# Performance work log

Hardware: AMD Instinct MI355X
Metric: run time of the kernel (lower is better)

Reference implementation:

```python
import jax, jax.numpy as jnp
import numpy as np

N, NB, D, F, E, NUM_RBF = 50000, 256, 128, 16, 800000, 15
EPS = 1e-7
NEG = 0.01
MAX_LEN = 5.0


def _glorot(k, shape):
    return jax.random.normal(k, shape, dtype=jnp.float32) / np.float32(np.sqrt(shape[0]))


def setup_inputs() -> dict:
    key = jax.random.key(0)
    ks = jax.random.split(key, 32)
    inp = {}
    inp['h_A'] = jax.random.normal(ks[0], (N, D), jnp.float32)
    inp['v_A'] = jax.random.normal(ks[1], (N, F, 3), jnp.float32)
    inp['x_A'] = jax.random.normal(ks[2], (N, 3), jnp.float32) * 3.0
    inp['h_B'] = jax.random.normal(ks[3], (NB, D), jnp.float32)
    inp['mask'] = jnp.ones((N, NB), jnp.float32)
    inp['src'] = jax.random.randint(ks[4], (E,), 0, N, dtype=jnp.int32)
    inp['dst'] = jax.random.randint(ks[5], (E,), 0, N, dtype=jnp.int32)
    inp['rbf_k'] = jnp.array([0.5], jnp.float32)
    inp['W_rbf1'] = _glorot(ks[6], (NUM_RBF, D)); inp['b_rbf1'] = jnp.zeros((D,), jnp.float32)
    inp['W_rbf2'] = _glorot(ks[7], (NUM_RBF, F)); inp['b_rbf2'] = jnp.zeros((F,), jnp.float32)
    inp['W_rbf3'] = _glorot(ks[8], (NUM_RBF, F)); inp['b_rbf3'] = jnp.zeros((F,), jnp.float32)
    inp['vn1_W'] = _glorot(ks[9], (F, F)); inp['vn1_U'] = _glorot(ks[10], (F, F))
    inp['vn2_W'] = _glorot(ks[11], (F, F)); inp['vn2_U'] = _glorot(ks[12], (F, F))
    inp['vn3_W'] = _glorot(ks[13], (F, F)); inp['vn3_U'] = _glorot(ks[14], (F, F))
    inp['phi1_W'] = _glorot(ks[15], (D + F, D)); inp['phi1_b'] = jnp.zeros((D,), jnp.float32)
    inp['phi2_W'] = _glorot(ks[16], (D + F, F)); inp['phi2_b'] = jnp.zeros((F,), jnp.float32)
    inp['phi3_W'] = _glorot(ks[17], (D, F)); inp['phi3_b'] = jnp.zeros((F,), jnp.float32)
    inp['Wq'] = _glorot(ks[18], (D, D)); inp['Wk'] = _glorot(ks[19], (D, D))
    inp['Wv'] = _glorot(ks[20], (D, D)); inp['bv'] = jnp.zeros((D,), jnp.float32)
    inp['gru_Wih'] = _glorot(ks[21], (3 * D, 2 * D)) * 0.5
    inp['gru_Whh'] = _glorot(ks[22], (3 * D, D)) * 0.5
    inp['gru_bih'] = jnp.zeros((3 * D,), jnp.float32)
    inp['gru_bhh'] = jnp.zeros((3 * D,), jnp.float32)
    inp['vmlp_W1'] = _glorot(ks[23], (2 * F, 2 * F)); inp['vmlp_U1'] = _glorot(ks[24], (2 * F, 2 * F))
    inp['vmlp_W2'] = _glorot(ks[25], (F, 2 * F))
    return inp


def _forward(h_A, v_A, x_A, h_B, mask, src, dst, rbf_k, W_rbf1, b_rbf1, W_rbf2, b_rbf2,
             W_rbf3, b_rbf3, vn1_W, vn1_U, vn2_W, vn2_U, vn3_W, vn3_U, phi1_W, phi1_b,
             phi2_W, phi2_b, phi3_W, phi3_b, Wq, Wk, Wv, bv, gru_Wih, gru_Whh, gru_bih,
             gru_bhh, vmlp_W1, vmlp_U1, vmlp_W2):
    lrelu = lambda x: jax.nn.leaky_relu(x, NEG)

    def vn_relu(v, W, U):  # Vector Neuron linear + VN-ReLU; v: [n, f, 3]
        q = jnp.einsum('gf,nfc->ngc', W, v)
        k = jnp.einsum('gf,nfc->ngc', U, v)
        dot = jnp.sum(q * k, -1, keepdims=True)
        ksq = jnp.sum(k * k, -1, keepdims=True) + EPS
        return jnp.where(dot >= 0, q, q - (dot / ksq) * k)

    # --- per-node mixed scalar/vector features (generate_mixed_features) ---
    vnorm1 = jnp.linalg.norm(vn_relu(v_A, vn1_W, vn1_U), axis=2) + EPS  # [N,F]
    vnorm2 = jnp.linalg.norm(vn_relu(v_A, vn2_W, vn2_U), axis=2) + EPS
    hp = lrelu(jnp.concatenate([h_A, vnorm1], 1) @ phi1_W + phi1_b)     # [N,D]
    hpp = lrelu(jnp.concatenate([h_A, vnorm2], 1) @ phi2_W + phi2_b)    # [N,F]
    vp = vn_relu(v_A, vn3_W, vn3_U) * lrelu(h_A @ phi3_W + phi3_b)[:, :, None]  # [N,F,3]

    # --- cross attention A <- B ---
    q = lrelu(h_A @ Wq)
    kk = lrelu(h_B @ Wk)
    vv = h_B @ Wv + bv
    a = mask * (q @ kk.T) - 1000.0 * (1.0 - mask)                       # [N,NB]
    attn = jax.nn.softmax(a, axis=1) @ vv                               # [N,D]

    # --- edge-wise RBF expansion + point convolution messages ---
    r_ij = x_A[src] - x_A[dst]                                          # [E,3]
    rnorm = jnp.linalg.norm(r_ij, axis=1, keepdims=True)                # [E,1]
    centers = jnp.linspace(0.0, MAX_LEN, NUM_RBF, dtype=jnp.float32)
    rbf = jnp.exp(-jnp.square(rnorm - centers) * rbf_k)                 # [E,R]
    rbf_h = rbf @ W_rbf1 + b_rbf1                                       # [E,D]
    rbf_v1 = rbf @ W_rbf2 + b_rbf2                                      # [E,F]
    rbf_v2 = rbf @ W_rbf3 + b_rbf3                                      # [E,F]
    msg_h = rbf_h * hp[dst]                                             # [E,D]
    # einsum('ef,ef,ec->efc', rbf_v2, hpp_dst, r_ij)
    msg_v = rbf_v1[:, :, None] * vp[dst] + (rbf_v2 * hpp[dst])[:, :, None] * r_ij[:, None, :]

    # --- mean aggregation at destination nodes (update_all copy_e + mean) ---
    n_nodes = h_A.shape[0]
    cnt = jax.ops.segment_sum(jnp.ones((src.shape[0],), msg_h.dtype), dst, num_segments=n_nodes)
    den = jnp.maximum(cnt, 1.0)
    agg_h = jax.ops.segment_sum(msg_h, dst, num_segments=n_nodes) / den[:, None]
    agg_v = jax.ops.segment_sum(msg_v, dst, num_segments=n_nodes) / den[:, None, None]

    # --- GRUCell(2D, D): input = [h, cross_attn], hidden = aggregated message ---
    x_in = jnp.concatenate([h_A, attn], -1)                             # [N,2D]
    gi = x_in @ gru_Wih.T + gru_bih
    gh = agg_h @ gru_Whh.T + gru_bhh
    Dh = h_A.shape[1]
    r = jax.nn.sigmoid(gi[:, :Dh] + gh[:, :Dh])
    z = jax.nn.sigmoid(gi[:, Dh:2 * Dh] + gh[:, Dh:2 * Dh])
    n = jnp.tanh(gi[:, 2 * Dh:] + r * gh[:, 2 * Dh:])
    node_upd = h_A + ((1.0 - z) * n + z * agg_h)

    # --- vector update via Vector_MLP(2F -> F) with residual ---
    vin = jnp.concatenate([v_A, agg_v], axis=1)                         # [N,2F,3]
    vh = vn_relu(vin, vmlp_W1, vmlp_U1)
    v_evolved = v_A + jnp.einsum('gf,nfc->ngc', vmlp_W2, vh)            # [N,F,3]
    return v_evolved, node_upd


def reference(h_A, v_A, x_A, h_B, mask, src, dst, rbf_k, W_rbf1, b_rbf1, W_rbf2, b_rbf2,
              W_rbf3, b_rbf3, vn1_W, vn1_U, vn2_W, vn2_U, vn3_W, vn3_U, phi1_W, phi1_b,
              phi2_W, phi2_b, phi3_W, phi3_b, Wq, Wk, Wv, bv, gru_Wih, gru_Whh, gru_bih,
              gru_bhh, vmlp_W1, vmlp_U1, vmlp_W2):
    return _forward(h_A, v_A, x_A, h_B, mask, src, dst, rbf_k, W_rbf1, b_rbf1, W_rbf2,
                    b_rbf2, W_rbf3, b_rbf3, vn1_W, vn1_U, vn2_W, vn2_U, vn3_W, vn3_U,
                    phi1_W, phi1_b, phi2_W, phi2_b, phi3_W, phi3_b, Wq, Wk, Wv, bv,
                    gru_Wih, gru_Whh, gru_bih, gru_bhh, vmlp_W1, vmlp_U1, vmlp_W2)
```

## Files before the change

kernel.cpp:

```cpp
#include <hip/hip_runtime.h>
#include <math.h>

#define NN 50000
#define NBB 256
#define DD 128
#define FF 16
#define EE 800000
#define RR 15
#define EPSV 1e-7f
#define CSPACE (5.0f/14.0f)

__device__ __forceinline__ float lrelu(float x){ return x >= 0.f ? x : 0.01f*x; }
__device__ __forceinline__ float sigmoidf_(float x){ return 1.f/(1.f+expf(-x)); }

typedef __bf16 bf16x8 __attribute__((ext_vector_type(8)));
typedef float f32x4 __attribute__((ext_vector_type(4)));

__device__ __forceinline__ unsigned short f2bf(float x){
    union { float f; unsigned int u; } a; a.f = x;
    unsigned int r = (a.u + 0x7fffu + ((a.u >> 16) & 1u)) >> 16;
    return (unsigned short)r;
}
__device__ __forceinline__ unsigned int pack2(float a, float b){
    return (unsigned int)f2bf(a) | ((unsigned int)f2bf(b) << 16);
}
__device__ __forceinline__ float bf2f(unsigned short v){
    union { unsigned int u; float f; } a; a.u = ((unsigned int)v) << 16; return a.f;
}
__device__ __forceinline__ bf16x8 ld8(const unsigned short* p){
    union { uint4 u; bf16x8 b; } x; x.u = *(const uint4*)p; return x.b;
}

__global__ void k_prep(const float* __restrict__ Wih, const float* __restrict__ Whh,
                       const float* __restrict__ Wq,
                       const float* __restrict__ phi1W, const float* __restrict__ phi2W,
                       const float* __restrict__ phi3W,
                       unsigned short* __restrict__ pWih, unsigned short* __restrict__ pWhh,
                       unsigned short* __restrict__ pWq,
                       unsigned short* __restrict__ pPhi1, unsigned short* __restrict__ pPhi2,
                       unsigned short* __restrict__ pPhi3){
    int i = blockIdx.x*256 + threadIdx.x;
    if (i < 3*8*8*64*8){
        int e = i&7, l=(i>>3)&63, kt=(i>>9)&7, c=(i>>12)&7, q=i>>15;
        int row = q*128 + c*16 + (l&15);
        int k = kt*32 + (l>>4)*8 + e;
        pWih[i] = f2bf(Wih[row*256 + k]);
    }
    if (i < 3*8*4*64*8){
        int e = i&7, l=(i>>3)&63, kt=(i>>9)&3, c=(i>>11)&7, q=i>>14;
        int row = q*128 + c*16 + (l&15);
        int k = kt*32 + (l>>4)*8 + e;
        pWhh[i] = f2bf(Whh[row*128 + k]);
    }
    if (i < 8*4*64*8){
        int e = i&7, l=(i>>3)&63, kt=(i>>9)&3, c=(i>>11)&7;
        pWq[i] = f2bf(Wq[(kt*32 + (l>>4)*8 + e)*DD + c*16 + (l&15)]);
    }
    if (i < 8*5*64*8){
        int e = i&7, l=(i>>3)&63;
        int t = i>>9;
        int kt = t%5, c = t/5;
        int k = kt*32 + (l>>4)*8 + e;
        int col = c*16 + (l&15);
        pPhi1[i] = f2bf(k < 144 ? phi1W[k*DD + col] : 0.f);
    }
    if (i < 5*64*8){
        int e = i&7, l=(i>>3)&63, kt = i>>9;
        int k = kt*32 + (l>>4)*8 + e;
        int col = l&15;
        pPhi2[i] = f2bf(k < 144 ? phi2W[k*FF + col] : 0.f);
    }
    if (i < 4*64*8){
        int e = i&7, l=(i>>3)&63, kt = i>>9;
        int k = kt*32 + (l>>4)*8 + e;
        int col = l&15;
        pPhi3[i] = f2bf(phi3W[k*FF + col]);
    }
}

__global__ __launch_bounds__(512) void k_node(
    const float* __restrict__ hA, const float* __restrict__ vA,
    const float* __restrict__ vn1W, const float* __restrict__ vn1U,
    const float* __restrict__ vn2W, const float* __restrict__ vn2U,
    const float* __restrict__ vn3W, const float* __restrict__ vn3U,
    const unsigned short* __restrict__ pPhi1, const float* __restrict__ phi1b,
    const unsigned short* __restrict__ pPhi2, const float* __restrict__ phi2b,
    const unsigned short* __restrict__ pPhi3, const float* __restrict__ phi3b,
    float* __restrict__ hpO, float* __restrict__ hppO, float* __restrict__ vpO)
{
    __shared__ unsigned short sH[64*128];
    __shared__ unsigned short sE[64*64];
    __shared__ float sVA[64*48];
    __shared__ float sO3[64*16*3];
    __shared__ float sW[6*256];
    int tid = threadIdx.x;
    int n0 = blockIdx.x*64;

    #pragma unroll
    for (int it = 0; it < 2; ++it){
        int c = tid + it*512;
        int row = c >> 4, cb = c & 15;
        int gn = n0 + row; if (gn > NN-1) gn = NN-1;
        const float* p = hA + (size_t)gn*DD + cb*8;
        float4 f0 = *(const float4*)p;
        float4 f1 = *(const float4*)(p+4);
        uint4 u;
        u.x = pack2(f0.x,f0.y); u.y = pack2(f0.z,f0.w);
        u.z = pack2(f1.x,f1.y); u.w = pack2(f1.z,f1.w);
        *(uint4*)&sH[row*128 + ((cb ^ (row&7))*8)] = u;
    }
    #pragma unroll
    for (int it = 0; it < 6; ++it){
        int i = tid + it*512;
        int row = i/48, cc = i%48;
        int gn = n0 + row; if (gn > NN-1) gn = NN-1;
        sVA[i] = vA[(size_t)gn*48 + cc];
    }
    #pragma unroll
    for (int it = 0; it < 3; ++it){
        int i = tid + it*512;
        float v;
        if      (i <  256) v = vn1W[i];
        else if (i <  512) v = vn1U[i-256];
        else if (i <  768) v = vn2W[i-512];
        else if (i < 1024) v = vn2U[i-768];
        else if (i < 1280) v = vn3W[i-1024];
        else               v = vn3U[i-1280];
        sW[i] = v;
    }
    {
        uint2* z = (uint2*)sE;
        z[tid] = make_uint2(0u,0u);
        z[tid+512] = make_uint2(0u,0u);
    }
    __syncthreads();

    #pragma unroll
    for (int it = 0; it < 2; ++it){
        int item = tid + it*512;
        int nl = item >> 4, g = item & 15;
        const float* v = &sVA[nl*48];
        float q0[3]={0,0,0}, q1[3]={0,0,0}, q2[3]={0,0,0};
        float c0[3]={0,0,0}, c1[3]={0,0,0}, c2[3]={0,0,0};
        #pragma unroll
        for (int ff = 0; ff < FF; ++ff){
            int fi = (ff + g) & 15;
            float v0 = v[fi*3], v1 = v[fi*3+1], v2 = v[fi*3+2];
            #pragma unroll
            for (int m = 0; m < 3; ++m){
                float w = sW[m*512 + g*16 + fi];
                float u = sW[m*512 + 256 + g*16 + fi];
                q0[m] += w*v0; q1[m] += w*v1; q2[m] += w*v2;
                c0[m] += u*v0; c1[m] += u*v1; c2[m] += u*v2;
            }
        }
        #pragma unroll
        for (int m = 0; m < 3; ++m){
            float dot = q0[m]*c0[m] + q1[m]*c1[m] + q2[m]*c2[m];
            float ksq = c0[m]*c0[m] + c1[m]*c1[m] + c2[m]*c2[m] + EPSV;
            float s = dot >= 0.f ? 0.f : dot/ksq;
            float o0 = q0[m]-s*c0[m], o1 = q1[m]-s*c1[m], o2 = q2[m]-s*c2[m];
            if (m < 2){
                float nr = sqrtf(o0*o0+o1*o1+o2*o2) + EPSV;
                int col = (m==0) ? g : (32+g);
                int cb = col>>3;
                sE[nl*64 + ((cb ^ (nl&7))*8) + (col&7)] = f2bf(nr);
            } else {
                float* o = &sO3[(nl*16+g)*3];
                o[0]=o0; o[1]=o1; o[2]=o2;
            }
        }
    }
    __syncthreads();

    int wv = tid>>6, l = tid&63, lr = l&15, lg = l>>4;

    f32x4 a1[4];
    #pragma unroll
    for (int rt = 0; rt < 4; ++rt) a1[rt] = (f32x4){0.f,0.f,0.f,0.f};
    for (int kt = 0; kt < 4; ++kt){
        bf16x8 b = ld8(pPhi1 + ((size_t)(wv*5+kt)*64 + l)*8);
        #pragma unroll
        for (int rt = 0; rt < 4; ++rt){
            int row = rt*16 + lr;
            bf16x8 a = ld8(&sH[row*128 + (((kt*4+lg) ^ (row&7))*8)]);
            a1[rt] = __builtin_amdgcn_mfma_f32_16x16x32_bf16(a, b, a1[rt], 0, 0, 0);
        }
    }
    {
        bf16x8 b = ld8(pPhi1 + ((size_t)(wv*5+4)*64 + l)*8);
        #pragma unroll
        for (int rt = 0; rt < 4; ++rt){
            int row = rt*16 + lr;
            bf16x8 a = ld8(&sE[row*64 + ((lg ^ (row&7))*8)]);
            a1[rt] = __builtin_amdgcn_mfma_f32_16x16x32_bf16(a, b, a1[rt], 0, 0, 0);
        }
    }
    f32x4 a23 = (f32x4){0.f,0.f,0.f,0.f};
    if (wv < 4){
        int row = wv*16 + lr;
        for (int kt = 0; kt < 4; ++kt){
            bf16x8 b = ld8(pPhi3 + ((size_t)kt*64 + l)*8);
            bf16x8 a = ld8(&sH[row*128 + (((kt*4+lg) ^ (row&7))*8)]);
            a23 = __builtin_amdgcn_mfma_f32_16x16x32_bf16(a, b, a23, 0, 0, 0);
        }
    } else {
        int row = (wv-4)*16 + lr;
        for (int kt = 0; kt < 4; ++kt){
            bf16x8 b = ld8(pPhi2 + ((size_t)kt*64 + l)*8);
            bf16x8 a = ld8(&sH[row*128 + (((kt*4+lg) ^ (row&7))*8)]);
            a23 = __builtin_amdgcn_mfma_f32_16x16x32_bf16(a, b, a23, 0, 0, 0);
        }
        {
            bf16x8 b = ld8(pPhi2 + ((size_t)4*64 + l)*8);
            bf16x8 a = ld8(&sE[row*64 + (((4+lg) ^ (row&7))*8)]);
            a23 = __builtin_amdgcn_mfma_f32_16x16x32_bf16(a, b, a23, 0, 0, 0);
        }
    }

    {
        int col = wv*16 + lr;
        float b1 = phi1b[col];
        #pragma unroll
        for (int rt = 0; rt < 4; ++rt){
            #pragma unroll
            for (int r4 = 0; r4 < 4; ++r4){
                int n = n0 + rt*16 + lg*4 + r4;
                if (n < NN) hpO[(size_t)n*DD + col] = lrelu(a1[rt][r4] + b1);
            }
        }
    }
    if (wv < 4){
        float b3 = phi3b[lr];
        #pragma unroll
        for (int r4 = 0; r4 < 4; ++r4){
            int nl = wv*16 + lg*4 + r4;
            int n = n0 + nl;
            float gate = lrelu(a23[r4] + b3);
            if (n < NN){
                const float* o = &sO3[(nl*16+lr)*3];
                float* vo = vpO + (size_t)n*48 + lr*3;
                vo[0] = o[0]*gate; vo[1] = o[1]*gate; vo[2] = o[2]*gate;
            }
        }
    } else {
        float b2 = phi2b[lr];
        #pragma unroll
        for (int r4 = 0; r4 < 4; ++r4){
            int nl = (wv-4)*16 + lg*4 + r4;
            int n = n0 + nl;
            if (n < NN) hppO[(size_t)n*FF + lr] = lrelu(a23[r4] + b2);
        }
    }
}

__global__ __launch_bounds__(128) void k_kv(
    const float* __restrict__ hB, const float* __restrict__ Wk,
    const float* __restrict__ Wv, const float* __restrict__ bv,
    unsigned short* __restrict__ pKK, unsigned short* __restrict__ pVV)
{
    __shared__ float sB[DD];
    int b = blockIdx.x, j = threadIdx.x;
    sB[j] = hB[(size_t)b*DD + j];
    __syncthreads();
    float ak = 0.f, av = bv[j];
    for (int i = 0; i < DD; ++i){
        float h = sB[i];
        ak += h*Wk[i*DD+j];
        av += h*Wv[i*DD+j];
    }
    {
        int c = b>>4, lr = b&15, kt = j>>5, lg = (j>>3)&3, e = j&7;
        pKK[((c*4+kt)*64 + lg*16 + lr)*8 + e] = f2bf(lrelu(ak));
    }
    {
        int kt = b>>5, lg = (b>>3)&3, e = b&7, c = j>>4, lr = j&15;
        pVV[((c*8+kt)*64 + lg*16 + lr)*8 + e] = f2bf(av);
    }
}

__global__ __launch_bounds__(512, 4) void k_attn_mfma(
    const float* __restrict__ hA, const unsigned short* __restrict__ pWq,
    const unsigned short* __restrict__ pKK, const unsigned short* __restrict__ pVV,
    const float* __restrict__ mask, float* __restrict__ attnO)
{
    __shared__ unsigned short sU[64*256];
    __shared__ float sMx[64][2];
    __shared__ float sSm[64][2];
    unsigned short* sX = sU;
    unsigned short* sQ = sU + 64*128;
    unsigned short* sP = sU;
    int tid = threadIdx.x;
    int n0 = blockIdx.x*64;

    #pragma unroll
    for (int it = 0; it < 2; ++it){
        int c = tid + it*512;
        int row = c >> 4, cb = c & 15;
        int gn = n0 + row; if (gn > NN-1) gn = NN-1;
        const float* srcp = hA + (size_t)gn*DD + cb*8;
        float4 f0 = *(const float4*)srcp;
        float4 f1 = *(const float4*)(srcp+4);
        uint4 u;
        u.x = pack2(f0.x,f0.y); u.y = pack2(f0.z,f0.w);
        u.z = pack2(f1.x,f1.y); u.w = pack2(f1.z,f1.w);
        *(uint4*)&sX[row*128 + ((cb ^ (row&7))*8)] = u;
    }
    __syncthreads();

    int wv = tid>>6, l = tid&63, lr = l&15, lg = l>>4;
    int rw = wv>>1, chh = wv&1;
    int rowA = rw*16 + lr;

    {
        f32x4 q[4];
        #pragma unroll
        for (int c = 0; c < 4; ++c) q[c] = (f32x4){0.f,0.f,0.f,0.f};
        for (int kt = 0; kt < 4; ++kt){
            bf16x8 a = ld8(&sX[rowA*128 + (((kt*4+lg) ^ (rowA&7))*8)]);
            #pragma unroll
            for (int c = 0; c < 4; ++c){
                bf16x8 b = ld8(pWq + (size_t)(((chh*4+c)*4 + kt)*512) + l*8);
                q[c] = __builtin_amdgcn_mfma_f32_16x16x32_bf16(a, b, q[c], 0, 0, 0);
            }
        }
        #pragma unroll
        for (int c = 0; c < 4; ++c)
        #pragma unroll
        for (int r4 = 0; r4 < 4; ++r4){
            int row = rw*16 + lg*4 + r4;
            int col = chh*64 + c*16 + lr;
            int cb = col>>3;
            sQ[row*128 + ((cb ^ (row&7))*8) + (col&7)] = f2bf(lrelu(q[c][r4]));
        }
    }
    __syncthreads();

    f32x4 S[8];
    #pragma unroll
    for (int cl = 0; cl < 8; ++cl) S[cl] = (f32x4){0.f,0.f,0.f,0.f};
    for (int kt = 0; kt < 4; ++kt){
        bf16x8 a = ld8(&sQ[rowA*128 + (((kt*4+lg) ^ (rowA&7))*8)]);
        #pragma unroll
        for (int cl = 0; cl < 8; ++cl){
            bf16x8 b = ld8(pKK + (size_t)(((chh*8+cl)*4 + kt)*512) + l*8);
            S[cl] = __builtin_amdgcn_mfma_f32_16x16x32_bf16(a, b, S[cl], 0, 0, 0);
        }
    }
    float den[4];
    #pragma unroll
    for (int r4 = 0; r4 < 4; ++r4){
        int row = rw*16 + lg*4 + r4;
        int gn = n0 + row; if (gn > NN-1) gn = NN-1;
        float mx = -1e30f;
        #pragma unroll
        for (int cl = 0; cl < 8; ++cl){
            int col = chh*128 + cl*16 + lr;
            float m = mask[(size_t)gn*NBB + col];
            float s = m*S[cl][r4] - 1000.f*(1.f-m);
            S[cl][r4] = s;
            mx = fmaxf(mx, s);
        }
        mx = fmaxf(mx, __shfl_xor(mx, 1));
        mx = fmaxf(mx, __shfl_xor(mx, 2));
        mx = fmaxf(mx, __shfl_xor(mx, 4));
        mx = fmaxf(mx, __shfl_xor(mx, 8));
        if (lr == 0) sMx[row][chh] = mx;
    }
    __syncthreads();
    #pragma unroll
    for (int r4 = 0; r4 < 4; ++r4){
        int row = rw*16 + lg*4 + r4;
        float m = fmaxf(sMx[row][0], sMx[row][1]);
        float sm = 0.f;
        #pragma unroll
        for (int cl = 0; cl < 8; ++cl){
            float p = expf(S[cl][r4] - m);
            S[cl][r4] = p;
            sm += p;
        }
        sm += __shfl_xor(sm, 1);
        sm += __shfl_xor(sm, 2);
        sm += __shfl_xor(sm, 4);
        sm += __shfl_xor(sm, 8);
        if (lr == 0) sSm[row][chh] = sm;
    }
    __syncthreads();
    #pragma unroll
    for (int r4 = 0; r4 < 4; ++r4){
        int row = rw*16 + lg*4 + r4;
        den[r4] = sSm[row][0] + sSm[row][1];
    }
    #pragma unroll
    for (int cl = 0; cl < 8; ++cl)
    #pragma unroll
    for (int r4 = 0; r4 < 4; ++r4){
        int row = rw*16 + lg*4 + r4;
        int col = chh*128 + cl*16 + lr;
        int cb = col>>3;
        sP[row*256 + ((cb ^ (row&7))*8) + (col&7)] = f2bf(S[cl][r4]);
    }
    __syncthreads();

    f32x4 O[4];
    #pragma unroll
    for (int c = 0; c < 4; ++c) O[c] = (f32x4){0.f,0.f,0.f,0.f};
    for (int kt = 0; kt < 8; ++kt){
        bf16x8 a = ld8(&sP[rowA*256 + (((kt*4+lg) ^ (rowA&7))*8)]);
        #pragma unroll
        for (int c = 0; c < 4; ++c){
            bf16x8 b = ld8(pVV + (size_t)(((chh*4+c)*8 + kt)*512) + l*8);
            O[c] = __builtin_amdgcn_mfma_f32_16x16x32_bf16(a, b, O[c], 0, 0, 0);
        }
    }
    #pragma unroll
    for (int c = 0; c < 4; ++c)
    #pragma unroll
    for (int r4 = 0; r4 < 4; ++r4){
        int row = rw*16 + lg*4 + r4;
        int n = n0 + row;
        if (n < NN){
            int col = chh*64 + c*16 + lr;
            attnO[(size_t)n*DD + col] = O[c][r4] / den[r4];
        }
    }
}

__global__ __launch_bounds__(256) void k_hist(const int* __restrict__ dst, int* __restrict__ deg){
    int e = blockIdx.x*256 + threadIdx.x;
    if (e < EE) atomicAdd(&deg[dst[e]], 1);
}

__global__ __launch_bounds__(256) void k_scan1(const int* __restrict__ deg,
                                               int* __restrict__ excl, int* __restrict__ bsum){
    __shared__ int s[256];
    int tid = threadIdx.x;
    int i = blockIdx.x*256 + tid;
    int v = (i < NN) ? deg[i] : 0;
    s[tid] = v;
    __syncthreads();
    for (int o = 1; o < 256; o <<= 1){
        int t = 0;
        if (tid >= o) t = s[tid-o];
        __syncthreads();
        if (tid >= o) s[tid] += t;
        __syncthreads();
    }
    if (i < NN) excl[i] = s[tid] - v;
    if (tid == 255) bsum[blockIdx.x] = s[255];
}

__global__ __launch_bounds__(256) void k_scan2(const int* __restrict__ bsum,
                                               int* __restrict__ boff, int nb){
    __shared__ int s[256];
    int tid = threadIdx.x;
    int v = (tid < nb) ? bsum[tid] : 0;
    s[tid] = v;
    __syncthreads();
    for (int o = 1; o < 256; o <<= 1){
        int t = 0;
        if (tid >= o) t = s[tid-o];
        __syncthreads();
        if (tid >= o) s[tid] += t;
        __syncthreads();
    }
    if (tid < nb) boff[tid] = s[tid] - v;
}

__global__ __launch_bounds__(256) void k_scan3(const int* __restrict__ excl,
                                               const int* __restrict__ boff,
                                               int* __restrict__ start, int* __restrict__ cursor){
    int i = blockIdx.x*256 + threadIdx.x;
    if (i < NN){
        int st = excl[i] + boff[blockIdx.x];
        start[i] = st;
        cursor[i] = st;
    }
    if (i == 0) start[NN] = EE;
}

__global__ __launch_bounds__(256) void k_scatter(const int* __restrict__ src,
                                                 const int* __restrict__ dst,
                                                 int* __restrict__ cursor, int* __restrict__ esrc){
    int e = blockIdx.x*256 + threadIdx.x;
    if (e >= EE) return;
    int pos = atomicAdd(&cursor[dst[e]], 1);
    esrc[pos] = src[e];
}

__global__ __launch_bounds__(256) void k_gather(const int* __restrict__ start,
                                                const int* __restrict__ esrc,
                                                const float* __restrict__ xA,
                                                const float* __restrict__ rbf_k,
                                                float* __restrict__ acc)
{
    int n = blockIdx.x*256 + threadIdx.x;
    if (n >= NN) return;
    float kc = rbf_k[0];
    float xd0 = xA[n*3+0], xd1 = xA[n*3+1], xd2 = xA[n*3+2];
    float a[64];
    #pragma unroll
    for (int i = 0; i < 64; ++i) a[i] = 0.f;
    int b0 = start[n], b1 = start[n+1];
    for (int i = b0; i < b1; ++i){
        int s = esrc[i];
        float r0 = xA[s*3+0]-xd0, r1 = xA[s*3+1]-xd1, r2 = xA[s*3+2]-xd2;
        float rn = sqrtf(r0*r0+r1*r1+r2*r2);
        a[0] += 1.f;
        a[16] += r0; a[17] += r1; a[18] += r2;
        #pragma unroll
        for (int q = 0; q < RR; ++q){
            float df = rn - (float)q*CSPACE;
            float rb = expf(-df*df*kc);
            a[1+q] += rb;
            a[19+q*3+0] += rb*r0;
            a[19+q*3+1] += rb*r1;
            a[19+q*3+2] += rb*r2;
        }
    }
    float4* o = (float4*)(acc + (size_t)n*64);
    #pragma unroll
    for (int i = 0; i < 16; ++i) o[i] = make_float4(a[4*i], a[4*i+1], a[4*i+2], a[4*i+3]);
}

__global__ __launch_bounds__(512) void k_gru_mfma(
    const float* __restrict__ hA, const float* __restrict__ attn,
    const float* __restrict__ hp, const float* __restrict__ acc,
    const float* __restrict__ Wr1, const float* __restrict__ br1,
    const unsigned short* __restrict__ pWih, const unsigned short* __restrict__ pWhh,
    const float* __restrict__ bih, const float* __restrict__ bhh,
    float* __restrict__ outNode)
{
    __shared__ unsigned short sX[64*256];
    __shared__ unsigned short sGm[64*128];
    int tid = threadIdx.x;
    int n0 = blockIdx.x*64;

    #pragma unroll
    for (int it = 0; it < 4; ++it){
        int c = tid + it*512;
        int row = c >> 5, cb = c & 31;
        int gn = n0 + row; if (gn > NN-1) gn = NN-1;
        int k = cb*8;
        const float* srcp = (k < DD) ? (hA + (size_t)gn*DD + k)
                                     : (attn + (size_t)gn*DD + (k-DD));
        float4 f0 = *(const float4*)srcp;
        float4 f1 = *(const float4*)(srcp+4);
        uint4 u;
        u.x = pack2(f0.x,f0.y); u.y = pack2(f0.z,f0.w);
        u.z = pack2(f1.x,f1.y); u.w = pack2(f1.z,f1.w);
        *(uint4*)&sX[row*256 + ((cb ^ (row&7))*8)] = u;
    }
    #pragma unroll
    for (int it = 0; it < 2; ++it){
        int c = tid + it*512;
        int row = c >> 4, cb = c & 15;
        int gn = n0 + row; if (gn > NN-1) gn = NN-1;
        int j = cb*8;
        const float* ar = acc + (size_t)gn*64;
        float cnt = ar[0];
        float den = fmaxf(cnt, 1.f);
        float s[8];
        #pragma unroll
        for (int e = 0; e < 8; ++e) s[e] = cnt*br1[j+e];
        #pragma unroll
        for (int r = 0; r < RR; ++r){
            float av = ar[1+r];
            #pragma unroll
            for (int e = 0; e < 8; ++e) s[e] += av*Wr1[r*DD + j + e];
        }
        float4 h0 = *(const float4*)(hp + (size_t)gn*DD + j);
        float4 h1 = *(const float4*)(hp + (size_t)gn*DD + j + 4);
        float g0 = h0.x*s[0]/den, g1 = h0.y*s[1]/den, g2 = h0.z*s[2]/den, g3 = h0.w*s[3]/den;
        float g4 = h1.x*s[4]/den, g5 = h1.y*s[5]/den, g6 = h1.z*s[6]/den, g7 = h1.w*s[7]/den;
        uint4 u;
        u.x = pack2(g0,g1); u.y = pack2(g2,g3); u.z = pack2(g4,g5); u.w = pack2(g6,g7);
        *(uint4*)&sGm[row*128 + ((cb ^ (row&7))*8)] = u;
    }
    __syncthreads();

    int wv = tid >> 6, l = tid & 63;
    int lr = l & 15, lg = l >> 4;

    f32x4 aR[4], aZ[4], aNI[4], aNH[4];
    #pragma unroll
    for (int rt = 0; rt < 4; ++rt){
        aR[rt] = (f32x4){0.f,0.f,0.f,0.f};
        aZ[rt] = (f32x4){0.f,0.f,0.f,0.f};
        aNI[rt] = (f32x4){0.f,0.f,0.f,0.f};
        aNH[rt] = (f32x4){0.f,0.f,0.f,0.f};
    }

    const unsigned short* bR = pWih + ((size_t)(0*8 + wv)*8)*512 + l*8;
    const unsigned short* bZ = pWih + ((size_t)(1*8 + wv)*8)*512 + l*8;
    const unsigned short* bN = pWih + ((size_t)(2*8 + wv)*8)*512 + l*8;
    for (int kt = 0; kt < 8; ++kt){
        bf16x8 br_ = ld8(bR + kt*512);
        bf16x8 bz_ = ld8(bZ + kt*512);
        bf16x8 bn_ = ld8(bN + kt*512);
        #pragma unroll
        for (int rt = 0; rt < 4; ++rt){
            int rowA = rt*16 + lr;
            bf16x8 a = ld8(&sX[rowA*256 + (((kt*4 + lg) ^ (rowA&7))*8)]);
            aR[rt]  = __builtin_amdgcn_mfma_f32_16x16x32_bf16(a, br_, aR[rt], 0, 0, 0);
            aZ[rt]  = __builtin_amdgcn_mfma_f32_16x16x32_bf16(a, bz_, aZ[rt], 0, 0, 0);
            aNI[rt] = __builtin_amdgcn_mfma_f32_16x16x32_bf16(a, bn_, aNI[rt], 0, 0, 0);
        }
    }
    const unsigned short* cR = pWhh + ((size_t)(0*8 + wv)*4)*512 + l*8;
    const unsigned short* cZ = pWhh + ((size_t)(1*8 + wv)*4)*512 + l*8;
    const unsigned short* cN = pWhh + ((size_t)(2*8 + wv)*4)*512 + l*8;
    for (int kt = 0; kt < 4; ++kt){
        bf16x8 br_ = ld8(cR + kt*512);
        bf16x8 bz_ = ld8(cZ + kt*512);
        bf16x8 bn_ = ld8(cN + kt*512);
        #pragma unroll
        for (int rt = 0; rt < 4; ++rt){
            int rowA = rt*16 + lr;
            bf16x8 a = ld8(&sGm[rowA*128 + (((kt*4 + lg) ^ (rowA&7))*8)]);
            aR[rt]  = __builtin_amdgcn_mfma_f32_16x16x32_bf16(a, br_, aR[rt], 0, 0, 0);
            aZ[rt]  = __builtin_amdgcn_mfma_f32_16x16x32_bf16(a, bz_, aZ[rt], 0, 0, 0);
            aNH[rt] = __builtin_amdgcn_mfma_f32_16x16x32_bf16(a, bn_, aNH[rt], 0, 0, 0);
        }
    }

    int col = wv*16 + lr;
    float b_r = bih[col] + bhh[col];
    float b_z = bih[DD+col] + bhh[DD+col];
    float b_ni = bih[2*DD+col];
    float b_nh = bhh[2*DD+col];
    #pragma unroll
    for (int rt = 0; rt < 4; ++rt){
        #pragma unroll
        for (int r4 = 0; r4 < 4; ++r4){
            int nl = rt*16 + lg*4 + r4;
            int n = n0 + nl;
            if (n < NN){
                float rg = sigmoidf_(aR[rt][r4] + b_r);
                float zg = sigmoidf_(aZ[rt][r4] + b_z);
                float ng = tanhf(aNI[rt][r4] + b_ni + rg*(aNH[rt][r4] + b_nh));
                float sg = bf2f(sGm[nl*128 + (((col>>3) ^ (nl&7))*8) + (col&7)]);
                float h = hA[(size_t)n*DD + col];
                outNode[(size_t)n*DD + col] = h + (1.f-zg)*ng + zg*sg;
            }
        }
    }
}

__global__ __launch_bounds__(256) void k_vec(
    const float* __restrict__ vA, const float* __restrict__ vp,
    const float* __restrict__ hpp, const float* __restrict__ acc,
    const float* __restrict__ Wr2, const float* __restrict__ br2,
    const float* __restrict__ Wr3, const float* __restrict__ br3,
    const float* __restrict__ W1, const float* __restrict__ U1,
    const float* __restrict__ W2, float* __restrict__ outV)
{
    __shared__ float sW1[32*32], sU1[32*32], sW2[16*32];
    __shared__ float sWr2[RR*FF], sWr3[RR*FF];
    __shared__ float sVin[8][32][3];
    __shared__ float sVh[8][32][3];
    __shared__ float sAcc[8][64];
    __shared__ float sVA[8][48];
    int tid = threadIdx.x;
    for (int i = tid; i < 1024; i += 256){ sW1[i]=W1[i]; sU1[i]=U1[i]; }
    for (int i = tid; i < 512; i += 256) sW2[i]=W2[i];
    for (int i = tid; i < RR*FF; i += 256){ sWr2[i]=Wr2[i]; sWr3[i]=Wr3[i]; }
    int n0 = blockIdx.x*8;
    for (int i = tid; i < 8*64; i += 256) sAcc[i/64][i%64] = acc[(size_t)n0*64 + i];
    for (int i = tid; i < 8*48; i += 256) sVA[i/48][i%48] = vA[(size_t)n0*48 + i];
    __syncthreads();
    int t = tid >> 5, g = tid & 31;
    int n = n0 + t;
    if (g < 16){
        int f = g;
        float cnt = sAcc[t][0];
        float den = fmaxf(cnt, 1.f);
        float s1 = cnt*br2[f];
        #pragma unroll
        for (int r = 0; r < RR; ++r) s1 += sAcc[t][1+r]*sWr2[r*FF+f];
        float hpv = hpp[(size_t)n*FF+f];
        float b3 = br3[f];
        #pragma unroll
        for (int c = 0; c < 3; ++c){
            float s2 = b3*sAcc[t][16+c];
            #pragma unroll
            for (int r = 0; r < RR; ++r) s2 += sAcc[t][19+r*3+c]*sWr3[r*FF+f];
            float aggv = (vp[(size_t)n*48 + f*3 + c]*s1 + hpv*s2)/den;
            sVin[t][FF+f][c] = aggv;
            sVin[t][f][c] = sVA[t][f*3+c];
        }
    }
    __syncthreads();
    {
        float q0=0,q1=0,q2=0,k0=0,k1=0,k2=0;
        #pragma unroll
        for (int ff = 0; ff < 32; ++ff){
            int f = (ff + g) & 31;
            float w = sW1[g*32+f], u = sU1[g*32+f];
            float v0=sVin[t][f][0], v1=sVin[t][f][1], v2=sVin[t][f][2];
            q0+=w*v0;q1+=w*v1;q2+=w*v2;
            k0+=u*v0;k1+=u*v1;k2+=u*v2;
        }
        float dot=q0*k0+q1*k1+q2*k2;
        float ksq=k0*k0+k1*k1+k2*k2+EPSV;
        float s = dot>=0.f?0.f:dot/ksq;
        sVh[t][g][0]=q0-s*k0; sVh[t][g][1]=q1-s*k1; sVh[t][g][2]=q2-s*k2;
    }
    __syncthreads();
    if (g < 16){
        float o0=sVA[t][g*3+0], o1=sVA[t][g*3+1], o2=sVA[t][g*3+2];
        #pragma unroll
        for (int ff = 0; ff < 32; ++ff){
            int f = (ff + g) & 31;
            float w = sW2[g*32+f];
            o0 += w*sVh[t][f][0];
            o1 += w*sVh[t][f][1];
            o2 += w*sVh[t][f][2];
        }
        outV[(size_t)n*48 + g*3 + 0] = o0;
        outV[(size_t)n*48 + g*3 + 1] = o1;
        outV[(size_t)n*48 + g*3 + 2] = o2;
    }
}

extern "C" void kernel_launch(void* const* d_in, const int* in_sizes, int n_in,
                              void* d_out, int out_size, void* d_ws, size_t ws_size,
                              hipStream_t stream)
{
    const float* hA   = (const float*)d_in[0];
    const float* vA   = (const float*)d_in[1];
    const float* xA   = (const float*)d_in[2];
    const float* hB   = (const float*)d_in[3];
    const float* mask = (const float*)d_in[4];
    const int*   src  = (const int*)d_in[5];
    const int*   dst  = (const int*)d_in[6];
    const float* rbfk = (const float*)d_in[7];
    const float* Wr1  = (const float*)d_in[8];
    const float* br1  = (const float*)d_in[9];
    const float* Wr2  = (const float*)d_in[10];
    const float* br2  = (const float*)d_in[11];
    const float* Wr3  = (const float*)d_in[12];
    const float* br3  = (const float*)d_in[13];
    const float* vn1W = (const float*)d_in[14];
    const float* vn1U = (const float*)d_in[15];
    const float* vn2W = (const float*)d_in[16];
    const float* vn2U = (const float*)d_in[17];
    const float* vn3W = (const float*)d_in[18];
    const float* vn3U = (const float*)d_in[19];
    const float* phi1W= (const float*)d_in[20];
    const float* phi1b= (const float*)d_in[21];
    const float* phi2W= (const float*)d_in[22];
    const float* phi2b= (const float*)d_in[23];
    const float* phi3W= (const float*)d_in[24];
    const float* phi3b= (const float*)d_in[25];
    const float* Wq   = (const float*)d_in[26];
    const float* Wk   = (const float*)d_in[27];
    const float* Wv   = (const float*)d_in[28];
    const float* bv   = (const float*)d_in[29];
    const float* Wih  = (const float*)d_in[30];
    const float* Whh  = (const float*)d_in[31];
    const float* bih  = (const float*)d_in[32];
    const float* bhh  = (const float*)d_in[33];
    const float* W1   = (const float*)d_in[34];
    const float* U1   = (const float*)d_in[35];
    const float* W2   = (const float*)d_in[36];

    float* ws = (float*)d_ws;
    float* hp     = ws;  ws += (size_t)NN*DD;
    float* hpp    = ws;  ws += (size_t)NN*FF;
    float* vp     = ws;  ws += (size_t)NN*FF*3;
    float* attn   = ws;  ws += (size_t)NN*DD;
    float* acc    = ws;  ws += (size_t)NN*64;
    unsigned short* pWih = (unsigned short*)ws; ws += (size_t)3*8*8*512/2;
    unsigned short* pWhh = (unsigned short*)ws; ws += (size_t)3*8*4*512/2;
    unsigned short* pWq  = (unsigned short*)ws; ws += (size_t)8*4*512/2;
    unsigned short* pKK  = (unsigned short*)ws; ws += (size_t)16*4*512/2;
    unsigned short* pVV  = (unsigned short*)ws; ws += (size_t)8*8*512/2;
    unsigned short* pPhi1= (unsigned short*)ws; ws += (size_t)8*5*512/2;
    unsigned short* pPhi2= (unsigned short*)ws; ws += (size_t)5*512/2;
    unsigned short* pPhi3= (unsigned short*)ws; ws += (size_t)4*512/2;
    int* deg    = (int*)ws;  ws += NN;
    int* excl   = (int*)ws;  ws += NN;
    int* bsum   = (int*)ws;  ws += 256;
    int* boff   = (int*)ws;  ws += 256;
    int* startN = (int*)ws;  ws += NN+1;
    int* cursor = (int*)ws;  ws += NN;
    int* esrc   = (int*)ws;  ws += EE;

    float* outV = (float*)d_out;
    float* outH = (float*)d_out + (size_t)NN*FF*3;

    const int NB_SCAN = (NN + 255)/256;

    hipMemsetAsync(deg, 0, (size_t)NN*sizeof(int), stream);
    k_prep<<<384, 256, 0, stream>>>(Wih, Whh, Wq, phi1W, phi2W, phi3W,
                                    pWih, pWhh, pWq, pPhi1, pPhi2, pPhi3);
    k_hist<<<(EE+255)/256, 256, 0, stream>>>(dst, deg);
    k_scan1<<<NB_SCAN, 256, 0, stream>>>(deg, excl, bsum);
    k_scan2<<<1, 256, 0, stream>>>(bsum, boff, NB_SCAN);
    k_scan3<<<NB_SCAN, 256, 0, stream>>>(excl, boff, startN, cursor);
    k_scatter<<<(EE+255)/256, 256, 0, stream>>>(src, dst, cursor, esrc);
    k_gather<<<(NN+255)/256, 256, 0, stream>>>(startN, esrc, xA, rbfk, acc);
    k_node<<<(NN+63)/64, 512, 0, stream>>>(hA, vA, vn1W, vn1U, vn2W, vn2U, vn3W, vn3U,
                                           pPhi1, phi1b, pPhi2, phi2b, pPhi3, phi3b,
                                           hp, hpp, vp);
    k_kv<<<NBB, 128, 0, stream>>>(hB, Wk, Wv, bv, pKK, pVV);
    k_attn_mfma<<<(NN+63)/64, 512, 0, stream>>>(hA, pWq, pKK, pVV, mask, attn);
    k_gru_mfma<<<(NN+63)/64, 512, 0, stream>>>(hA, attn, hp, acc, Wr1, br1,
                                               pWih, pWhh, bih, bhh, outH);
    k_vec<<<NN/8, 256, 0, stream>>>(vA, vp, hpp, acc, Wr2, br2, Wr3, br3, W1, U1, W2, outV);
}
```

Baseline: 379.8 us.

## Fuse attention into GRU kernel and split gather edges across four lanes

```diff
diff --git a/kernel.cpp b/kernel.cpp
--- a/kernel.cpp
+++ b/kernel.cpp
@@ -279,32 +279,36 @@
     }
 }
 
-__global__ __launch_bounds__(512, 4) void k_attn_mfma(
+__global__ __launch_bounds__(512) void k_ag(
     const float* __restrict__ hA, const unsigned short* __restrict__ pWq,
     const unsigned short* __restrict__ pKK, const unsigned short* __restrict__ pVV,
-    const float* __restrict__ mask, float* __restrict__ attnO)
+    const float* __restrict__ mask,
+    const float* __restrict__ hp, const float* __restrict__ acc,
+    const float* __restrict__ Wr1, const float* __restrict__ br1,
+    const unsigned short* __restrict__ pWih, const unsigned short* __restrict__ pWhh,
+    const float* __restrict__ bih, const float* __restrict__ bhh,
+    float* __restrict__ outNode)
 {
-    __shared__ unsigned short sU[64*256];
-    __shared__ float sMx[64][2];
-    __shared__ float sSm[64][2];
-    unsigned short* sX = sU;
-    unsigned short* sQ = sU + 64*128;
-    unsigned short* sP = sU;
+    __shared__ unsigned short sXG[64*256];
+    __shared__ unsigned short sP[64*256];
+    __shared__ unsigned short sQG[64*128];
     int tid = threadIdx.x;
     int n0 = blockIdx.x*64;
+    float* sMx = (float*)sP;
+    float* sSm = (float*)sP + 128;
 
     #pragma unroll
     for (int it = 0; it < 2; ++it){
         int c = tid + it*512;
         int row = c >> 4, cb = c & 15;
         int gn = n0 + row; if (gn > NN-1) gn = NN-1;
-        const float* srcp = hA + (size_t)gn*DD + cb*8;
-        float4 f0 = *(const float4*)srcp;
-        float4 f1 = *(const float4*)(srcp+4);
+        const float* p = hA + (size_t)gn*DD + cb*8;
+        float4 f0 = *(const float4*)p;
+        float4 f1 = *(const float4*)(p+4);
         uint4 u;
         u.x = pack2(f0.x,f0.y); u.y = pack2(f0.z,f0.w);
         u.z = pack2(f1.x,f1.y); u.w = pack2(f1.z,f1.w);
-        *(uint4*)&sX[row*128 + ((cb ^ (row&7))*8)] = u;
+        *(uint4*)&sXG[row*256 + ((cb ^ (row&7))*8)] = u;
     }
     __syncthreads();
 
@@ -317,13 +321,14 @@
         #pragma unroll
         for (int c = 0; c < 4; ++c) q[c] = (f32x4){0.f,0.f,0.f,0.f};
         for (int kt = 0; kt < 4; ++kt){
-            bf16x8 a = ld8(&sX[rowA*128 + (((kt*4+lg) ^ (rowA&7))*8)]);
+            bf16x8 a = ld8(&sXG[rowA*256 + (((kt*4+lg) ^ (rowA&7))*8)]);
             #pragma unroll
             for (int c = 0; c < 4; ++c){
                 bf16x8 b = ld8(pWq + (size_t)(((chh*4+c)*4 + kt)*512) + l*8);
                 q[c] = __builtin_amdgcn_mfma_f32_16x16x32_bf16(a, b, q[c], 0, 0, 0);
             }
         }
+        __syncthreads();
         #pragma unroll
         for (int c = 0; c < 4; ++c)
         #pragma unroll
@@ -331,7 +336,7 @@
             int row = rw*16 + lg*4 + r4;
             int col = chh*64 + c*16 + lr;
             int cb = col>>3;
-            sQ[row*128 + ((cb ^ (row&7))*8) + (col&7)] = f2bf(lrelu(q[c][r4]));
+            sQG[row*128 + ((cb ^ (row&7))*8) + (col&7)] = f2bf(lrelu(q[c][r4]));
         }
     }
     __syncthreads();
@@ -340,7 +345,7 @@
     #pragma unroll
     for (int cl = 0; cl < 8; ++cl) S[cl] = (f32x4){0.f,0.f,0.f,0.f};
     for (int kt = 0; kt < 4; ++kt){
-        bf16x8 a = ld8(&sQ[rowA*128 + (((kt*4+lg) ^ (rowA&7))*8)]);
+        bf16x8 a = ld8(&sQG[rowA*128 + (((kt*4+lg) ^ (rowA&7))*8)]);
         #pragma unroll
         for (int cl = 0; cl < 8; ++cl){
             bf16x8 b = ld8(pKK + (size_t)(((chh*8+cl)*4 + kt)*512) + l*8);
@@ -365,13 +370,13 @@
         mx = fmaxf(mx, __shfl_xor(mx, 2));
         mx = fmaxf(mx, __shfl_xor(mx, 4));
         mx = fmaxf(mx, __shfl_xor(mx, 8));
-        if (lr == 0) sMx[row][chh] = mx;
+        if (lr == 0) sMx[row*2+chh] = mx;
     }
     __syncthreads();
     #pragma unroll
     for (int r4 = 0; r4 < 4; ++r4){
         int row = rw*16 + lg*4 + r4;
-        float m = fmaxf(sMx[row][0], sMx[row][1]);
+        float m = fmaxf(sMx[row*2+0], sMx[row*2+1]);
         float sm = 0.f;
         #pragma unroll
         for (int cl = 0; cl < 8; ++cl){
@@ -383,14 +388,16 @@
         sm += __shfl_xor(sm, 2);
         sm += __shfl_xor(sm, 4);
         sm += __shfl_xor(sm, 8);
-        if (lr == 0) sSm[row][chh] = sm;
+        if (lr == 0) sSm[row*2+chh] = sm;
     }
     __syncthreads();
     #pragma unroll
     for (int r4 = 0; r4 < 4; ++r4){
         int row = rw*16 + lg*4 + r4;
-        den[r4] = sSm[row][0] + sSm[row][1];
-    }
+        den[r4] = sSm[row*2+0] + sSm[row*2+1];
+    }
+    __syncthreads();
+
     #pragma unroll
     for (int cl = 0; cl < 8; ++cl)
     #pragma unroll
@@ -400,28 +407,121 @@
         int cb = col>>3;
         sP[row*256 + ((cb ^ (row&7))*8) + (col&7)] = f2bf(S[cl][r4]);
     }
-    __syncthreads();
-
-    f32x4 O[4];
-    #pragma unroll
-    for (int c = 0; c < 4; ++c) O[c] = (f32x4){0.f,0.f,0.f,0.f};
+    {
+        int c = tid;
+        int row = c >> 3, cb = c & 7;
+        #pragma unroll
+        for (int it = 0; it < 2; ++it){
+            int cc = tid + it*512;
+            row = cc >> 4; cb = cc & 15;
+            int gn = n0 + row; if (gn > NN-1) gn = NN-1;
+            int j = cb*8;
+            const float* ar = acc + (size_t)gn*64;
+            float cnt = ar[0];
+            float dn = fmaxf(cnt, 1.f);
+            float s[8];
+            #pragma unroll
+            for (int e = 0; e < 8; ++e) s[e] = cnt*br1[j+e];
+            #pragma unroll
+            for (int r = 0; r < RR; ++r){
+                float av = ar[1+r];
+                #pragma unroll
+                for (int e = 0; e < 8; ++e) s[e] += av*Wr1[r*DD + j + e];
+            }
+            float4 h0 = *(const float4*)(hp + (size_t)gn*DD + j);
+            float4 h1 = *(const float4*)(hp + (size_t)gn*DD + j + 4);
+            float g0 = h0.x*s[0]/dn, g1 = h0.y*s[1]/dn, g2 = h0.z*s[2]/dn, g3 = h0.w*s[3]/dn;
+            float g4 = h1.x*s[4]/dn, g5 = h1.y*s[5]/dn, g6 = h1.z*s[6]/dn, g7 = h1.w*s[7]/dn;
+            uint4 u;
+            u.x = pack2(g0,g1); u.y = pack2(g2,g3); u.z = pack2(g4,g5); u.w = pack2(g6,g7);
+            *(uint4*)&sQG[row*128 + ((cb ^ (row&7))*8)] = u;
+        }
+    }
+    __syncthreads();
+
+    {
+        f32x4 O[4];
+        #pragma unroll
+        for (int c = 0; c < 4; ++c) O[c] = (f32x4){0.f,0.f,0.f,0.f};
+        for (int kt = 0; kt < 8; ++kt){
+            bf16x8 a = ld8(&sP[rowA*256 + (((kt*4+lg) ^ (rowA&7))*8)]);
+            #pragma unroll
+            for (int c = 0; c < 4; ++c){
+                bf16x8 b = ld8(pVV + (size_t)(((chh*4+c)*8 + kt)*512) + l*8);
+                O[c] = __builtin_amdgcn_mfma_f32_16x16x32_bf16(a, b, O[c], 0, 0, 0);
+            }
+        }
+        #pragma unroll
+        for (int c = 0; c < 4; ++c)
+        #pragma unroll
+        for (int r4 = 0; r4 < 4; ++r4){
+            int row = rw*16 + lg*4 + r4;
+            int colg = 128 + chh*64 + c*16 + lr;
+            int cb = colg>>3;
+            sXG[row*256 + ((cb ^ (row&7))*8) + (colg&7)] = f2bf(O[c][r4] / den[r4]);
+        }
+    }
+    __syncthreads();
+
+    f32x4 aR[4], aZ[4], aNI[4], aNH[4];
+    #pragma unroll
+    for (int rt = 0; rt < 4; ++rt){
+        aR[rt] = (f32x4){0.f,0.f,0.f,0.f};
+        aZ[rt] = (f32x4){0.f,0.f,0.f,0.f};
+        aNI[rt] = (f32x4){0.f,0.f,0.f,0.f};
+        aNH[rt] = (f32x4){0.f,0.f,0.f,0.f};
+    }
+    const unsigned short* bR = pWih + ((size_t)(0*8 + wv)*8)*512 + l*8;
+    const unsigned short* bZ = pWih + ((size_t)(1*8 + wv)*8)*512 + l*8;
+    const unsigned short* bN = pWih + ((size_t)(2*8 + wv)*8)*512 + l*8;
     for (int kt = 0; kt < 8; ++kt){
-        bf16x8 a = ld8(&sP[rowA*256 + (((kt*4+lg) ^ (rowA&7))*8)]);
-        #pragma unroll
-        for (int c = 0; c < 4; ++c){
-            bf16x8 b = ld8(pVV + (size_t)(((chh*4+c)*8 + kt)*512) + l*8);
-            O[c] = __builtin_amdgcn_mfma_f32_16x16x32_bf16(a, b, O[c], 0, 0, 0);
-        }
-    }
-    #pragma unroll
-    for (int c = 0; c < 4; ++c)
-    #pragma unroll
-    for (int r4 = 0; r4 < 4; ++r4){
-        int row = rw*16 + lg*4 + r4;
-        int n = n0 + row;
-        if (n < NN){
-            int col = chh*64 + c*16 + lr;
-            attnO[(size_t)n*DD + col] = O[c][r4] / den[r4];
+        bf16x8 br_ = ld8(bR + kt*512);
+        bf16x8 bz_ = ld8(bZ + kt*512);
+        bf16x8 bn_ = ld8(bN + kt*512);
+        #pragma unroll
+        for (int rt = 0; rt < 4; ++rt){
+            int rA = rt*16 + lr;
+            bf16x8 a = ld8(&sXG[rA*256 + (((kt*4 + lg) ^ (rA&7))*8)]);
+            aR[rt]  = __builtin_amdgcn_mfma_f32_16x16x32_bf16(a, br_, aR[rt], 0, 0, 0);
+            aZ[rt]  = __builtin_amdgcn_mfma_f32_16x16x32_bf16(a, bz_, aZ[rt], 0, 0, 0);
+            aNI[rt] = __builtin_amdgcn_mfma_f32_16x16x32_bf16(a, bn_, aNI[rt], 0, 0, 0);
+        }
+    }
+    const unsigned short* cR = pWhh + ((size_t)(0*8 + wv)*4)*512 + l*8;
+    const unsigned short* cZ = pWhh + ((size_t)(1*8 + wv)*4)*512 + l*8;
+    const unsigned short* cN = pWhh + ((size_t)(2*8 + wv)*4)*512 + l*8;
+    for (int kt = 0; kt < 4; ++kt){
+        bf16x8 br_ = ld8(cR + kt*512);
+        bf16x8 bz_ = ld8(cZ + kt*512);
+        bf16x8 bn_ = ld8(cN + kt*512);
+        #pragma unroll
+        for (int rt = 0; rt < 4; ++rt){
+            int rA = rt*16 + lr;
+            bf16x8 a = ld8(&sQG[rA*128 + (((kt*4 + lg) ^ (rA&7))*8)]);
+            aR[rt]  = __builtin_amdgcn_mfma_f32_16x16x32_bf16(a, br_, aR[rt], 0, 0, 0);
+            aZ[rt]  = __builtin_amdgcn_mfma_f32_16x16x32_bf16(a, bz_, aZ[rt], 0, 0, 0);
+            aNH[rt] = __builtin_amdgcn_mfma_f32_16x16x32_bf16(a, bn_, aNH[rt], 0, 0, 0);
+        }
+    }
+    int col = wv*16 + lr;
+    float b_r = bih[col] + bhh[col];
+    float b_z = bih[DD+col] + bhh[DD+col];
+    float b_ni = bih[2*DD+col];
+    float b_nh = bhh[2*DD+col];
+    #pragma unroll
+    for (int rt = 0; rt < 4; ++rt){
+        #pragma unroll
+        for (int r4 = 0; r4 < 4; ++r4){
+            int nl = rt*16 + lg*4 + r4;
+            int n = n0 + nl;
+            if (n < NN){
+                float rg = sigmoidf_(aR[rt][r4] + b_r);
+                float zg = sigmoidf_(aZ[rt][r4] + b_z);
+                float ng = tanhf(aNI[rt][r4] + b_ni + rg*(aNH[rt][r4] + b_nh));
+                float sg = bf2f(sQG[nl*128 + (((col>>3) ^ (nl&7))*8) + (col&7)]);
+                float h = hA[(size_t)n*DD + col];
+                outNode[(size_t)n*DD + col] = h + (1.f-zg)*ng + zg*sg;
+            }
         }
     }
 }
@@ -494,7 +594,8 @@
                                                 const float* __restrict__ rbf_k,
                                                 float* __restrict__ acc)
 {
-    int n = blockIdx.x*256 + threadIdx.x;
+    int gt = blockIdx.x*256 + threadIdx.x;
+    int n = gt >> 2, sub = gt & 3;
     if (n >= NN) return;
     float kc = rbf_k[0];
     float xd0 = xA[n*3+0], xd1 = xA[n*3+1], xd2 = xA[n*3+2];
@@ -502,7 +603,7 @@
     #pragma unroll
     for (int i = 0; i < 64; ++i) a[i] = 0.f;
     int b0 = start[n], b1 = start[n+1];
-    for (int i = b0; i < b1; ++i){
+    for (int i = b0 + sub; i < b1; i += 4){
         int s = esrc[i];
         float r0 = xA[s*3+0]-xd0, r1 = xA[s*3+1]-xd1, r2 = xA[s*3+2]-xd2;
         float rn = sqrtf(r0*r0+r1*r1+r2*r2);
@@ -518,132 +619,16 @@
             a[19+q*3+2] += rb*r2;
         }
     }
+    #pragma unroll
+    for (int i = 0; i < 64; ++i){
+        a[i] += __shfl_xor(a[i], 1);
+        a[i] += __shfl_xor(a[i], 2);
+    }
     float4* o = (float4*)(acc + (size_t)n*64);
     #pragma unroll
-    for (int i = 0; i < 16; ++i) o[i] = make_float4(a[4*i], a[4*i+1], a[4*i+2], a[4*i+3]);
-}
-
-__global__ __launch_bounds__(512) void k_gru_mfma(
-    const float* __restrict__ hA, const float* __restrict__ attn,
-    const float* __restrict__ hp, const float* __restrict__ acc,
-    const float* __restrict__ Wr1, const float* __restrict__ br1,
-    const unsigned short* __restrict__ pWih, const unsigned short* __restrict__ pWhh,
-    const float* __restrict__ bih, const float* __restrict__ bhh,
-    float* __restrict__ outNode)
-{
-    __shared__ unsigned short sX[64*256];
-    __shared__ unsigned short sGm[64*128];
-    int tid = threadIdx.x;
-    int n0 = blockIdx.x*64;
-
-    #pragma unroll
-    for (int it = 0; it < 4; ++it){
-        int c = tid + it*512;
-        int row = c >> 5, cb = c & 31;
-        int gn = n0 + row; if (gn > NN-1) gn = NN-1;
-        int k = cb*8;
-        const float* srcp = (k < DD) ? (hA + (size_t)gn*DD + k)
-                                     : (attn + (size_t)gn*DD + (k-DD));
-        float4 f0 = *(const float4*)srcp;
-        float4 f1 = *(const float4*)(srcp+4);
-        uint4 u;
-        u.x = pack2(f0.x,f0.y); u.y = pack2(f0.z,f0.w);
-        u.z = pack2(f1.x,f1.y); u.w = pack2(f1.z,f1.w);
-        *(uint4*)&sX[row*256 + ((cb ^ (row&7))*8)] = u;
-    }
-    #pragma unroll
-    for (int it = 0; it < 2; ++it){
-        int c = tid + it*512;
-        int row = c >> 4, cb = c & 15;
-        int gn = n0 + row; if (gn > NN-1) gn = NN-1;
-        int j = cb*8;
-        const float* ar = acc + (size_t)gn*64;
-        float cnt = ar[0];
-        float den = fmaxf(cnt, 1.f);
-        float s[8];
-        #pragma unroll
-        for (int e = 0; e < 8; ++e) s[e] = cnt*br1[j+e];
-        #pragma unroll
-        for (int r = 0; r < RR; ++r){
-            float av = ar[1+r];
-            #pragma unroll
-            for (int e = 0; e < 8; ++e) s[e] += av*Wr1[r*DD + j + e];
-        }
-        float4 h0 = *(const float4*)(hp + (size_t)gn*DD + j);
-        float4 h1 = *(const float4*)(hp + (size_t)gn*DD + j + 4);
-        float g0 = h0.x*s[0]/den, g1 = h0.y*s[1]/den, g2 = h0.z*s[2]/den, g3 = h0.w*s[3]/den;
-        float g4 = h1.x*s[4]/den, g5 = h1.y*s[5]/den, g6 = h1.z*s[6]/den, g7 = h1.w*s[7]/den;
-        uint4 u;
-        u.x = pack2(g0,g1); u.y = pack2(g2,g3); u.z = pack2(g4,g5); u.w = pack2(g6,g7);
-        *(uint4*)&sGm[row*128 + ((cb ^ (row&7))*8)] = u;
-    }
-    __syncthreads();
-
-    int wv = tid >> 6, l = tid & 63;
-    int lr = l & 15, lg = l >> 4;
-
-    f32x4 aR[4], aZ[4], aNI[4], aNH[4];
-    #pragma unroll
-    for (int rt = 0; rt < 4; ++rt){
-        aR[rt] = (f32x4){0.f,0.f,0.f,0.f};
-        aZ[rt] = (f32x4){0.f,0.f,0.f,0.f};
-        aNI[rt] = (f32x4){0.f,0.f,0.f,0.f};
-        aNH[rt] = (f32x4){0.f,0.f,0.f,0.f};
-    }
-
-    const unsigned short* bR = pWih + ((size_t)(0*8 + wv)*8)*512 + l*8;
-    const unsigned short* bZ = pWih + ((size_t)(1*8 + wv)*8)*512 + l*8;
-    const unsigned short* bN = pWih + ((size_t)(2*8 + wv)*8)*512 + l*8;
-    for (int kt = 0; kt < 8; ++kt){
-        bf16x8 br_ = ld8(bR + kt*512);
-        bf16x8 bz_ = ld8(bZ + kt*512);
-        bf16x8 bn_ = ld8(bN + kt*512);
-        #pragma unroll
-        for (int rt = 0; rt < 4; ++rt){
-            int rowA = rt*16 + lr;
-            bf16x8 a = ld8(&sX[rowA*256 + (((kt*4 + lg) ^ (rowA&7))*8)]);
-            aR[rt]  = __builtin_amdgcn_mfma_f32_16x16x32_bf16(a, br_, aR[rt], 0, 0, 0);
-            aZ[rt]  = __builtin_amdgcn_mfma_f32_16x16x32_bf16(a, bz_, aZ[rt], 0, 0, 0);
-            aNI[rt] = __builtin_amdgcn_mfma_f32_16x16x32_bf16(a, bn_, aNI[rt], 0, 0, 0);
-        }
-    }
-    const unsigned short* cR = pWhh + ((size_t)(0*8 + wv)*4)*512 + l*8;
-    const unsigned short* cZ = pWhh + ((size_t)(1*8 + wv)*4)*512 + l*8;
-    const unsigned short* cN = pWhh + ((size_t)(2*8 + wv)*4)*512 + l*8;
-    for (int kt = 0; kt < 4; ++kt){
-        bf16x8 br_ = ld8(cR + kt*512);
-        bf16x8 bz_ = ld8(cZ + kt*512);
-        bf16x8 bn_ = ld8(cN + kt*512);
-        #pragma unroll
-        for (int rt = 0; rt < 4; ++rt){
-            int rowA = rt*16 + lr;
-            bf16x8 a = ld8(&sGm[rowA*128 + (((kt*4 + lg) ^ (rowA&7))*8)]);
-            aR[rt]  = __builtin_amdgcn_mfma_f32_16x16x32_bf16(a, br_, aR[rt], 0, 0, 0);
-            aZ[rt]  = __builtin_amdgcn_mfma_f32_16x16x32_bf16(a, bz_, aZ[rt], 0, 0, 0);
-            aNH[rt] = __builtin_amdgcn_mfma_f32_16x16x32_bf16(a, bn_, aNH[rt], 0, 0, 0);
-        }
-    }
-
-    int col = wv*16 + lr;
-    float b_r = bih[col] + bhh[col];
-    float b_z = bih[DD+col] + bhh[DD+col];
-    float b_ni = bih[2*DD+col];
-    float b_nh = bhh[2*DD+col];
-    #pragma unroll
-    for (int rt = 0; rt < 4; ++rt){
-        #pragma unroll
-        for (int r4 = 0; r4 < 4; ++r4){
-            int nl = rt*16 + lg*4 + r4;
-            int n = n0 + nl;
-            if (n < NN){
-                float rg = sigmoidf_(aR[rt][r4] + b_r);
-                float zg = sigmoidf_(aZ[rt][r4] + b_z);
-                float ng = tanhf(aNI[rt][r4] + b_ni + rg*(aNH[rt][r4] + b_nh));
-                float sg = bf2f(sGm[nl*128 + (((col>>3) ^ (nl&7))*8) + (col&7)]);
-                float h = hA[(size_t)n*DD + col];
-                outNode[(size_t)n*DD + col] = h + (1.f-zg)*ng + zg*sg;
-            }
-        }
+    for (int i = 0; i < 4; ++i){
+        int idx = sub*4 + i;
+        o[idx] = make_float4(a[4*idx], a[4*idx+1], a[4*idx+2], a[4*idx+3]);
     }
 }
 
@@ -769,7 +754,6 @@
     float* hp     = ws;  ws += (size_t)NN*DD;
     float* hpp    = ws;  ws += (size_t)NN*FF;
     float* vp     = ws;  ws += (size_t)NN*FF*3;
-    float* attn   = ws;  ws += (size_t)NN*DD;
     float* acc    = ws;  ws += (size_t)NN*64;
     unsigned short* pWih = (unsigned short*)ws; ws += (size_t)3*8*8*512/2;
     unsigned short* pWhh = (unsigned short*)ws; ws += (size_t)3*8*4*512/2;
@@ -800,13 +784,12 @@
     k_scan2<<<1, 256, 0, stream>>>(bsum, boff, NB_SCAN);
     k_scan3<<<NB_SCAN, 256, 0, stream>>>(excl, boff, startN, cursor);
     k_scatter<<<(EE+255)/256, 256, 0, stream>>>(src, dst, cursor, esrc);
-    k_gather<<<(NN+255)/256, 256, 0, stream>>>(startN, esrc, xA, rbfk, acc);
+    k_gather<<<(NN*4+255)/256, 256, 0, stream>>>(startN, esrc, xA, rbfk, acc);
     k_node<<<(NN+63)/64, 512, 0, stream>>>(hA, vA, vn1W, vn1U, vn2W, vn2U, vn3W, vn3U,
                                            pPhi1, phi1b, pPhi2, phi2b, pPhi3, phi3b,
                                            hp, hpp, vp);
     k_kv<<<NBB, 128, 0, stream>>>(hB, Wk, Wv, bv, pKK, pVV);
-    k_attn_mfma<<<(NN+63)/64, 512, 0, stream>>>(hA, pWq, pKK, pVV, mask, attn);
-    k_gru_mfma<<<(NN+63)/64, 512, 0, stream>>>(hA, attn, hp, acc, Wr1, br1,
-                                               pWih, pWhh, bih, bhh, outH);
+    k_ag<<<(NN+63)/64, 512, 0, stream>>>(hA, pWq, pKK, pVV, mask, hp, acc, Wr1, br1,
+                                         pWih, pWhh, bih, bhh, outH);
     k_vec<<<NN/8, 256, 0, stream>>>(vA, vp, hpp, acc, Wr2, br2, Wr3, br3, W1, U1, W2, outV);
 }
```

New measurement: 442.1 us. 1.16x slower.
